# Kernel optimization log

Hardware: AMD Instinct MI355X
Metric: run time of the kernel (lower is better)

Reference implementation:

```python
import jax, jax.numpy as jnp
import numpy as np

N, E, IN_C, HID, OUT_C = 50000, 800000, 128, 64, 64
NEG_SLOPE = 0.2
BN_EPS = 1e-5


def _gat(x, edges, W, a_src, a_dst, b):
    """PyG-style GATConv: linear -> per-head attention logits -> softmax over
    incoming edges (self-loops added, as in PyG default) -> weighted scatter-add."""
    n = x.shape[0]
    H, C = a_src.shape
    xw = (x @ W).reshape(n, H, C)                      # [N,H,C]
    loop = jnp.arange(n)
    src = jnp.concatenate([edges[0], loop])            # [E+N]
    dst = jnp.concatenate([edges[1], loop])
    al_s = jnp.sum(xw * a_src, axis=-1)                # [N,H]
    al_d = jnp.sum(xw * a_dst, axis=-1)
    e = jax.nn.leaky_relu(al_s[src] + al_d[dst], NEG_SLOPE)   # [E+N,H]
    emax = jax.ops.segment_max(e, dst, num_segments=n)        # stable softmax per target
    w = jnp.exp(e - emax[dst])
    denom = jax.ops.segment_sum(w, dst, num_segments=n)
    alpha = w / (denom[dst] + 1e-16)                   # [E+N,H]
    msg = xw[src] * alpha[:, :, None]                  # [E+N,H,C]
    out = jax.ops.segment_sum(msg, dst, num_segments=n)       # [N,H,C]
    return out.reshape(n, H * C) + b


def _bn(x, g, be):
    # BatchNorm1d training-mode forward: biased batch statistics over nodes.
    m = jnp.mean(x, axis=0)
    v = jnp.mean((x - m) ** 2, axis=0)
    return (x - m) * jax.lax.rsqrt(v + BN_EPS) * g + be


def setup_inputs() -> dict:
    key = jax.random.key(0)
    ks = jax.random.split(key, 20)
    p = lambda k, s: (jax.random.normal(k, s, jnp.float32) * 0.1)
    return {
        "x": jax.random.normal(ks[0], (1, N, IN_C), jnp.float32),
        "adj": jax.random.randint(ks[1], (2, E), 0, N),
        # conv1: in=128 -> hidden=64, heads=2 (concat -> 128)
        "W1": p(ks[2], (IN_C, 2 * HID)), "as1": p(ks[3], (2, HID)), "ad1": p(ks[4], (2, HID)), "b1": jnp.zeros((2 * HID,), jnp.float32),
        "g1": jnp.ones((2 * HID,), jnp.float32), "be1": jnp.zeros((2 * HID,), jnp.float32),
        # conv2: 128 -> 64, heads=2
        "W2": p(ks[5], (2 * HID, 2 * HID)), "as2": p(ks[6], (2, HID)), "ad2": p(ks[7], (2, HID)), "b2": jnp.zeros((2 * HID,), jnp.float32),
        "g2": jnp.ones((2 * HID,), jnp.float32), "be2": jnp.zeros((2 * HID,), jnp.float32),
        # conv3: 128 -> 64, heads=1
        "W3": p(ks[8], (2 * HID, OUT_C)), "as3": p(ks[9], (1, OUT_C)), "ad3": p(ks[10], (1, OUT_C)), "b3": jnp.zeros((OUT_C,), jnp.float32),
        "g3": jnp.ones((OUT_C,), jnp.float32), "be3": jnp.zeros((OUT_C,), jnp.float32),
    }


def reference(x, adj, W1, as1, ad1, b1, g1, be1, W2, as2, ad2, b2, g2, be2, W3, as3, ad3, b3, g3, be3):
    x0 = x[0]                                          # squeeze batch dim
    x1 = _bn(jax.nn.relu(_gat(x0, adj, W1, as1, ad1, b1)), g1, be1)   # [N,128]
    x2 = _bn(jax.nn.relu(_gat(x1, adj, W2, as2, ad2, b2)), g2, be2)   # [N,128]
    x3 = _bn(jax.nn.relu(_gat(x2, adj, W3, as3, ad3, b3)), g3, be3)   # [N,64]
    return jnp.concatenate([x1, x2, x3], axis=-1)      # [N,320]
```

## Files before the change

kernel.cpp:

```cpp
#include <hip/hip_runtime.h>

typedef unsigned int uint;
typedef unsigned short ushort;


static __device__ __forceinline__ ushort bf16_rne(float x) {
    uint u = __float_as_uint(x);
    return (ushort)((u + 0x7fffu + ((u >> 16) & 1u)) >> 16);
}
static __device__ __forceinline__ float bf16_f(ushort h) {
    return __uint_as_float(((uint)h) << 16);
}

__global__ __launch_bounds__(256) void k_bcount(const int* __restrict__ dst, int e,
                                                int* __restrict__ bcntp) {
    __shared__ int h[512];
    int tid = threadIdx.x;
    h[tid] = 0;
    h[tid + 256] = 0;
    __syncthreads();
    int stride = gridDim.x * 256;
    for (int i = blockIdx.x * 256 + tid; i < e; i += stride)
        atomicAdd(&h[dst[i] >> 7], 1);
    __syncthreads();
    if (h[tid]) atomicAdd(&bcntp[tid * 16], h[tid]);
    if (h[tid + 256]) atomicAdd(&bcntp[(tid + 256) * 16], h[tid + 256]);
}

__global__ __launch_bounds__(512) void k_bscan(const int* __restrict__ bcntp,
                                               int* __restrict__ bbase,
                                               int* __restrict__ bcurp, int nb, int n,
                                               int total, int* __restrict__ row_start) {
    __shared__ int s[512];
    int tid = threadIdx.x;
    int v = 0;
    if (tid < nb) v = bcntp[tid * 16] + min(128, n - (tid << 7));
    s[tid] = v;
    __syncthreads();
    for (int off = 1; off < 512; off <<= 1) {
        int t = (tid >= off) ? s[tid - off] : 0;
        __syncthreads();
        s[tid] += t;
        __syncthreads();
    }
    if (tid < nb) {
        int excl = s[tid] - v;
        bbase[tid] = excl;
        bcurp[tid * 16] = excl;
    }
    if (tid == 0) {
        bbase[nb] = total;
        row_start[n] = total;
    }
}

__global__ __launch_bounds__(512) void k_bscatter(const int* __restrict__ src,
                                                  const int* __restrict__ dst, int e, int n,
                                                  int* __restrict__ bcurp,
                                                  int* __restrict__ pk) {
    __shared__ int hcnt[512], bstart[512], bcursor[512], gbase[512];
    __shared__ int stage[8192];
    int tid = threadIdx.x;
    int total = e + n;
    int nchunk = (total + 8191) >> 13;
    for (int c = blockIdx.x; c < nchunk; c += gridDim.x) {
        int base = c << 13;
        int cnt = min(8192, total - base);
        hcnt[tid] = 0;
        __syncthreads();
        for (int j = tid; j < cnt; j += 512) {
            int i = base + j;
            int d = (i < e) ? dst[i] : (i - e);
            atomicAdd(&hcnt[d >> 7], 1);
        }
        __syncthreads();
        int v = hcnt[tid];
        bstart[tid] = v;
        __syncthreads();
        for (int off = 1; off < 512; off <<= 1) {
            int t = (tid >= off) ? bstart[tid - off] : 0;
            __syncthreads();
            bstart[tid] += t;
            __syncthreads();
        }
        int excl = bstart[tid] - v;
        __syncthreads();
        bstart[tid] = excl;
        bcursor[tid] = excl;
        if (v) gbase[tid] = atomicAdd(&bcurp[tid * 16], v);
        __syncthreads();
        for (int j = tid; j < cnt; j += 512) {
            int i = base + j;
            int d, sv;
            if (i < e) { d = dst[i]; sv = src[i]; }
            else       { d = i - e; sv = d; }
            uint b = (uint)(d >> 7);
            int r = atomicAdd(&bcursor[b], 1);
            stage[r] = (int)((b << 23) | ((uint)(d & 127) << 16) | (uint)sv);
        }
        __syncthreads();
        for (int j = tid; j < cnt; j += 512) {
            int p = stage[j];
            int b = (int)(((uint)p) >> 23);
            pk[gbase[b] + (j - bstart[b])] = p;
        }
        __syncthreads();
    }
}

__global__ __launch_bounds__(256) void k_bfill(const int* __restrict__ pk,
                                               const int* __restrict__ bbase, int n,
                                               int* __restrict__ row_start,
                                               int* __restrict__ col) {
    int b = blockIdx.x;
    int s0 = bbase[b], s1 = bbase[b + 1];
    int seg = s1 - s0;
    int node0 = b << 7;
    int nn = min(128, n - node0);
    int tid = threadIdx.x;
    __shared__ int cnt[128], scn[128];
    __shared__ int colst[4608];
    if (tid < 128) cnt[tid] = 0;
    __syncthreads();
    for (int j = tid; j < seg; j += 256)
        atomicAdd(&cnt[(pk[s0 + j] >> 16) & 127], 1);
    __syncthreads();
    int myc = 0;
    if (tid < 128) { myc = cnt[tid]; scn[tid] = myc; }
    __syncthreads();
    for (int off = 1; off < 128; off <<= 1) {
        int t = (tid >= off && tid < 128) ? scn[tid - off] : 0;
        __syncthreads();
        if (tid < 128) scn[tid] += t;
        __syncthreads();
    }
    int excl = 0;
    if (tid < 128) excl = scn[tid] - myc;
    if (tid < nn) row_start[node0 + tid] = s0 + excl;
    __syncthreads();
    if (tid < 128) cnt[tid] = excl;
    __syncthreads();
    bool big = seg > 4608;
    for (int j = tid; j < seg; j += 256) {
        int p = pk[s0 + j];
        int r = atomicAdd(&cnt[(p >> 16) & 127], 1);
        if (big) col[s0 + r] = p & 0xffff;
        else colst[r] = p & 0xffff;
    }
    if (!big) {
        __syncthreads();
        for (int j = tid; j < seg; j += 256) col[s0 + j] = colst[j];
    }
}

typedef __attribute__((ext_vector_type(8))) short short8;
typedef __attribute__((ext_vector_type(4))) float float4v;

template <int F, int H, bool BN>
__global__ __launch_bounds__(256) void k_gemm(const float* __restrict__ A,
                                              const float* __restrict__ W,
                                              const float* __restrict__ sc,
                                              const float* __restrict__ sh,
                                              const float* __restrict__ asrc,
                                              const float* __restrict__ adst,
                                              ushort* __restrict__ xwb,
                                              float* __restrict__ al_s,
                                              float* __restrict__ al_d, int M) {
    constexpr int K = 128;
    constexpr int NT = F / 16;
    __shared__ __align__(16) ushort Ahi[64][40], Alo[64][40];
    __shared__ __align__(16) ushort Whi[F][40], Wlo[F][40];
    int tid = threadIdx.x;
    int wave = tid >> 6, lane = tid & 63;
    int quad = lane >> 4, l15 = lane & 15;
    int rowBase = blockIdx.x * 64;

    float4v acc[NT];
#pragma unroll
    for (int t = 0; t < NT; t++) acc[t] = (float4v){0.f, 0.f, 0.f, 0.f};

    for (int k0 = 0; k0 < K; k0 += 32) {
        {
            int kk = tid & 31, rg = tid >> 5;
            float scv = BN ? sc[k0 + kk] : 1.f;
            float shv = BN ? sh[k0 + kk] : 0.f;
#pragma unroll
            for (int i = 0; i < 8; i++) {
                int r = rg + i * 8;
                int grow = rowBase + r;
                float a = (grow < M) ? A[(long long)grow * K + k0 + kk] : 0.f;
                if (BN) a = fmaf(a, scv, shv);
                ushort hi = bf16_rne(a);
                ushort lo = bf16_rne(a - bf16_f(hi));
                Ahi[r][kk] = hi;
                Alo[r][kk] = lo;
            }
        }
        if (F == 128) {
            int n = tid & 127, kg = tid >> 7;
#pragma unroll
            for (int j = 0; j < 16; j++) {
                int kk = kg + j * 2;
                float w = W[(long long)(k0 + kk) * F + n];
                ushort hi = bf16_rne(w);
                ushort lo = bf16_rne(w - bf16_f(hi));
                Whi[n][kk] = hi;
                Wlo[n][kk] = lo;
            }
        } else {
            int n = tid & 63, kg = tid >> 6;
#pragma unroll
            for (int j = 0; j < 8; j++) {
                int kk = kg + j * 4;
                float w = W[(long long)(k0 + kk) * F + n];
                ushort hi = bf16_rne(w);
                ushort lo = bf16_rne(w - bf16_f(hi));
                Whi[n][kk] = hi;
                Wlo[n][kk] = lo;
            }
        }
        __syncthreads();

        short8 ah = *(const short8*)&Ahi[wave * 16 + l15][quad * 8];
        short8 al = *(const short8*)&Alo[wave * 16 + l15][quad * 8];
#pragma unroll
        for (int t = 0; t < NT; t++) {
            short8 bh = *(const short8*)&Whi[t * 16 + l15][quad * 8];
            short8 bl = *(const short8*)&Wlo[t * 16 + l15][quad * 8];
            acc[t] = __builtin_amdgcn_mfma_f32_16x16x32_bf16(ah, bh, acc[t], 0, 0, 0);
            acc[t] = __builtin_amdgcn_mfma_f32_16x16x32_bf16(ah, bl, acc[t], 0, 0, 0);
            acc[t] = __builtin_amdgcn_mfma_f32_16x16x32_bf16(al, bh, acc[t], 0, 0, 0);
        }
        __syncthreads();
    }

    float asl[NT], adl[NT];
#pragma unroll
    for (int t = 0; t < NT; t++) {
        asl[t] = asrc[t * 16 + l15];
        adl[t] = adst[t * 16 + l15];
    }
#pragma unroll
    for (int r = 0; r < 4; r++) {
        int grow = rowBase + wave * 16 + quad * 4 + r;
        if (grow < M) {
#pragma unroll
            for (int t = 0; t < NT; t++)
                xwb[(long long)grow * F + t * 16 + l15] = bf16_rne(acc[t][r]);
        }
        float ps0 = 0.f, pd0 = 0.f, ps1 = 0.f, pd1 = 0.f;
#pragma unroll
        for (int t = 0; t < NT; t++) {
            float v = acc[t][r];
            if (H == 2 && t >= NT / 2) {
                ps1 = fmaf(v, asl[t], ps1);
                pd1 = fmaf(v, adl[t], pd1);
            } else {
                ps0 = fmaf(v, asl[t], ps0);
                pd0 = fmaf(v, adl[t], pd0);
            }
        }
#pragma unroll
        for (int off = 1; off < 16; off <<= 1) {
            ps0 += __shfl_xor(ps0, off);
            pd0 += __shfl_xor(pd0, off);
            if (H == 2) {
                ps1 += __shfl_xor(ps1, off);
                pd1 += __shfl_xor(pd1, off);
            }
        }
        if (l15 == 0 && grow < M) {
            al_s[grow * H + 0] = ps0;
            al_d[grow * H + 0] = pd0;
            if (H == 2) {
                al_s[grow * H + 1] = ps1;
                al_d[grow * H + 1] = pd1;
            }
        }
    }
}

template <int F, int H>
__global__ __launch_bounds__(256) void k_agg(const uint* __restrict__ xwb,
                      const float* __restrict__ al_s,
                      const float* __restrict__ al_d, const int* __restrict__ row_start,
                      const int* __restrict__ col, const float* __restrict__ bias,
                      float* __restrict__ y, int n) {
    int wid = (blockIdx.x * blockDim.x + threadIdx.x) >> 6;
    int lane = threadIdx.x & 63;
    if (wid >= n) return;
    int beg = row_start[wid], end = row_start[wid + 1];

    float ald[H];
#pragma unroll
    for (int h = 0; h < H; h++) ald[h] = al_d[wid * H + h];

    if (end - beg <= 64) {
        int nb = end - beg;
        int s_c = 0;
        float ev0 = -1e30f, ev1 = -1e30f;
        if (lane < nb) {
            s_c = col[beg + lane];
            if (H == 2) {
                float2 av = ((const float2*)al_s)[s_c];
                float e0 = av.x + ald[0];
                float e1 = av.y + ald[1];
                ev0 = (e0 >= 0.f) ? e0 : 0.2f * e0;
                ev1 = (e1 >= 0.f) ? e1 : 0.2f * e1;
            } else {
                float e0 = al_s[s_c] + ald[0];
                ev0 = (e0 >= 0.f) ? e0 : 0.2f * e0;
            }
        }
        float m0 = ev0, m1 = ev1;
#pragma unroll
        for (int off = 32; off; off >>= 1) {
            m0 = fmaxf(m0, __shfl_xor(m0, off));
            if (H == 2) m1 = fmaxf(m1, __shfl_xor(m1, off));
        }
        float x0 = (lane < nb) ? __expf(ev0 - m0) : 0.f;
        float x1 = (H == 2 && lane < nb) ? __expf(ev1 - m1) : 0.f;
        float l0 = x0, l1 = x1;
#pragma unroll
        for (int off = 32; off; off >>= 1) {
            l0 += __shfl_xor(l0, off);
            if (H == 2) l1 += __shfl_xor(l1, off);
        }
        float a0 = x0 / (l0 + 1e-16f);
        float a1 = (H == 2) ? x1 / (l1 + 1e-16f) : a0;

        float accv0 = 0.f, accv1 = 0.f, accv2 = 0.f, accv3 = 0.f;
        const uint2* xw2 = (const uint2*)xwb;

        if (F == 128) {
            int li = lane & 31;
            int half = lane >> 5;
            bool head0 = (li < 16);
            for (int j = 0; j < nb; j += 16) {
                int rr[8];
                float alq[8];
#pragma unroll
                for (int q = 0; q < 8; q++) {
                    int e = j + 2 * q + half;
                    rr[q] = __shfl(s_c, e);
                    float aa = __shfl(a0, e);
                    float bb = __shfl(a1, e);
                    alq[q] = (H == 2) ? (head0 ? aa : bb) : aa;
                }
                uint2 uu[8];
#pragma unroll
                for (int q = 0; q < 8; q++)
                    uu[q] = xw2[(rr[q] << 5) + li];
#pragma unroll
                for (int q = 0; q < 8; q++) {
                    accv0 = fmaf(alq[q], __uint_as_float(uu[q].x << 16), accv0);
                    accv1 = fmaf(alq[q], __uint_as_float(uu[q].x & 0xffff0000u), accv1);
                    accv2 = fmaf(alq[q], __uint_as_float(uu[q].y << 16), accv2);
                    accv3 = fmaf(alq[q], __uint_as_float(uu[q].y & 0xffff0000u), accv3);
                }
            }
            accv0 += __shfl_xor(accv0, 32);
            accv1 += __shfl_xor(accv1, 32);
            accv2 += __shfl_xor(accv2, 32);
            accv3 += __shfl_xor(accv3, 32);
            if (li == lane) {
                float4 o;
                o.x = fmaxf(accv0 + bias[4 * li + 0], 0.f);
                o.y = fmaxf(accv1 + bias[4 * li + 1], 0.f);
                o.z = fmaxf(accv2 + bias[4 * li + 2], 0.f);
                o.w = fmaxf(accv3 + bias[4 * li + 3], 0.f);
                ((float4*)y)[(long long)wid * 32 + li] = o;
            }
        } else {
            int li = lane & 15;
            int g = lane >> 4;
            for (int j = 0; j < nb; j += 32) {
                int rr[8];
                float alq[8];
#pragma unroll
                for (int q = 0; q < 8; q++) {
                    int e = j + 4 * q + g;
                    rr[q] = __shfl(s_c, e);
                    alq[q] = __shfl(a0, e);
                }
                uint2 uu[8];
#pragma unroll
                for (int q = 0; q < 8; q++)
                    uu[q] = xw2[(rr[q] << 4) + li];
#pragma unroll
                for (int q = 0; q < 8; q++) {
                    accv0 = fmaf(alq[q], __uint_as_float(uu[q].x << 16), accv0);
                    accv1 = fmaf(alq[q], __uint_as_float(uu[q].x & 0xffff0000u), accv1);
                    accv2 = fmaf(alq[q], __uint_as_float(uu[q].y << 16), accv2);
                    accv3 = fmaf(alq[q], __uint_as_float(uu[q].y & 0xffff0000u), accv3);
                }
            }
            accv0 += __shfl_xor(accv0, 16); accv0 += __shfl_xor(accv0, 32);
            accv1 += __shfl_xor(accv1, 16); accv1 += __shfl_xor(accv1, 32);
            accv2 += __shfl_xor(accv2, 16); accv2 += __shfl_xor(accv2, 32);
            accv3 += __shfl_xor(accv3, 16); accv3 += __shfl_xor(accv3, 32);
            if (lane < 16) {
                float4 o;
                o.x = fmaxf(accv0 + bias[4 * li + 0], 0.f);
                o.y = fmaxf(accv1 + bias[4 * li + 1], 0.f);
                o.z = fmaxf(accv2 + bias[4 * li + 2], 0.f);
                o.w = fmaxf(accv3 + bias[4 * li + 3], 0.f);
                ((float4*)y)[(long long)wid * 16 + li] = o;
            }
        }
        return;
    }

    float acc0 = 0.f, acc1 = 0.f;
    {
        float m[H], l[H];
#pragma unroll
        for (int h = 0; h < H; h++) {
            m[h] = -1e30f;
            l[h] = 0.f;
        }
        for (int e = beg + lane; e < end; e += 64) {
            int s = col[e];
#pragma unroll
            for (int h = 0; h < H; h++) {
                float ev = al_s[s * H + h] + ald[h];
                ev = (ev >= 0.f) ? ev : 0.2f * ev;
                if (ev > m[h]) {
                    l[h] = l[h] * __expf(m[h] - ev) + 1.f;
                    m[h] = ev;
                } else {
                    l[h] += __expf(ev - m[h]);
                }
            }
        }
#pragma unroll
        for (int off = 32; off; off >>= 1) {
#pragma unroll
            for (int h = 0; h < H; h++) {
                float mo = __shfl_xor(m[h], off);
                float lo = __shfl_xor(l[h], off);
                float mn = fmaxf(m[h], mo);
                l[h] = l[h] * __expf(m[h] - mn) + lo * __expf(mo - mn);
                m[h] = mn;
            }
        }
        float inv[H];
#pragma unroll
        for (int h = 0; h < H; h++) inv[h] = 1.f / (l[h] + 1e-16f);

        for (int base = beg; base < end; base += 64) {
            int nb = min(64, end - base);
            int ec = min(base + lane, end - 1);
            int s = col[ec];
            float a0, a1;
            {
                float av[H];
#pragma unroll
                for (int h = 0; h < H; h++) {
                    float ev = al_s[s * H + h] + ald[h];
                    ev = (ev >= 0.f) ? ev : 0.2f * ev;
                    av[h] = __expf(ev - m[h]) * inv[h];
                }
                a0 = av[0];
                a1 = av[H - 1];
            }
            int j = 0;
            for (; j + 4 <= nb; j += 4) {
                int s0 = __shfl(s, j + 0), s1 = __shfl(s, j + 1);
                int s2 = __shfl(s, j + 2), s3 = __shfl(s, j + 3);
                float q00 = __shfl(a0, j + 0), q01 = __shfl(a1, j + 0);
                float q10 = __shfl(a0, j + 1), q11 = __shfl(a1, j + 1);
                float q20 = __shfl(a0, j + 2), q21 = __shfl(a1, j + 2);
                float q30 = __shfl(a0, j + 3), q31 = __shfl(a1, j + 3);
                float p0, p1, p2, p3;
                if (H == 2) {
                    p0 = (lane < 32) ? q00 : q01;
                    p1 = (lane < 32) ? q10 : q11;
                    p2 = (lane < 32) ? q20 : q21;
                    p3 = (lane < 32) ? q30 : q31;
                } else {
                    p0 = q00; p1 = q10; p2 = q20; p3 = q30;
                }
                if (F == 128) {
                    uint u0 = xwb[(s0 << 6) + lane];
                    uint u1 = xwb[(s1 << 6) + lane];
                    uint u2 = xwb[(s2 << 6) + lane];
                    uint u3 = xwb[(s3 << 6) + lane];
                    acc0 = fmaf(p0, __uint_as_float(u0 << 16), acc0);
                    acc1 = fmaf(p0, __uint_as_float(u0 & 0xffff0000u), acc1);
                    acc0 = fmaf(p1, __uint_as_float(u1 << 16), acc0);
                    acc1 = fmaf(p1, __uint_as_float(u1 & 0xffff0000u), acc1);
                    acc0 = fmaf(p2, __uint_as_float(u2 << 16), acc0);
                    acc1 = fmaf(p2, __uint_as_float(u2 & 0xffff0000u), acc1);
                    acc0 = fmaf(p3, __uint_as_float(u3 << 16), acc0);
                    acc1 = fmaf(p3, __uint_as_float(u3 & 0xffff0000u), acc1);
                } else {
                    int idx = lane >> 1;
                    bool hi = (lane & 1) != 0;
                    uint u0 = xwb[(s0 << 5) + idx];
                    uint u1 = xwb[(s1 << 5) + idx];
                    uint u2 = xwb[(s2 << 5) + idx];
                    uint u3 = xwb[(s3 << 5) + idx];
                    acc0 = fmaf(p0, __uint_as_float(hi ? (u0 & 0xffff0000u) : (u0 << 16)), acc0);
                    acc0 = fmaf(p1, __uint_as_float(hi ? (u1 & 0xffff0000u) : (u1 << 16)), acc0);
                    acc0 = fmaf(p2, __uint_as_float(hi ? (u2 & 0xffff0000u) : (u2 << 16)), acc0);
                    acc0 = fmaf(p3, __uint_as_float(hi ? (u3 & 0xffff0000u) : (u3 << 16)), acc0);
                }
            }
            for (; j < nb; ++j) {
                int sj = __shfl(s, j);
                float q0 = __shfl(a0, j);
                float q1 = __shfl(a1, j);
                float alpha;
                if (H == 2) {
                    alpha = (lane < 32) ? q0 : q1;
                } else {
                    alpha = q0;
                }
                if (F == 128) {
                    uint u = xwb[(sj << 6) + lane];
                    acc0 = fmaf(alpha, __uint_as_float(u << 16), acc0);
                    acc1 = fmaf(alpha, __uint_as_float(u & 0xffff0000u), acc1);
                } else {
                    uint u = xwb[(sj << 5) + (lane >> 1)];
                    acc0 = fmaf(alpha, __uint_as_float((lane & 1) ? (u & 0xffff0000u) : (u << 16)), acc0);
                }
            }
        }
    }

    if (F == 128) {
        float2 o;
        o.x = fmaxf(acc0 + bias[2 * lane], 0.f);
        o.y = fmaxf(acc1 + bias[2 * lane + 1], 0.f);
        ((float2*)y)[(long long)wid * 64 + lane] = o;
    } else {
        y[(long long)wid * 64 + lane] = fmaxf(acc0 + bias[lane], 0.f);
    }
}

template <int F>
__global__ void k_bn_stats(const float* __restrict__ y, float* __restrict__ sums, int n) {
    constexpr int C4 = F / 4;
    constexpr int NPB = 256 / C4;
    int c4 = threadIdx.x % C4;
    int sub = threadIdx.x / C4;
    float4 s = {0, 0, 0, 0}, s2 = {0, 0, 0, 0};
    for (int node = blockIdx.x * NPB + sub; node < n; node += gridDim.x * NPB) {
        float4 v = ((const float4*)y)[node * C4 + c4];
        s.x += v.x; s.y += v.y; s.z += v.z; s.w += v.w;
        s2.x += v.x * v.x; s2.y += v.y * v.y; s2.z += v.z * v.z; s2.w += v.w * v.w;
    }
    __shared__ float4 ls[256], ls2[256];
    ls[threadIdx.x] = s;
    ls2[threadIdx.x] = s2;
    __syncthreads();
    if (sub == 0) {
#pragma unroll
        for (int k = 1; k < NPB; k++) {
            float4 t = ls[c4 + k * C4], t2 = ls2[c4 + k * C4];
            s.x += t.x; s.y += t.y; s.z += t.z; s.w += t.w;
            s2.x += t2.x; s2.y += t2.y; s2.z += t2.z; s2.w += t2.w;
        }
        atomicAdd(&sums[c4 * 4 + 0], s.x);
        atomicAdd(&sums[c4 * 4 + 1], s.y);
        atomicAdd(&sums[c4 * 4 + 2], s.z);
        atomicAdd(&sums[c4 * 4 + 3], s.w);
        atomicAdd(&sums[F + c4 * 4 + 0], s2.x);
        atomicAdd(&sums[F + c4 * 4 + 1], s2.y);
        atomicAdd(&sums[F + c4 * 4 + 2], s2.z);
        atomicAdd(&sums[F + c4 * 4 + 3], s2.w);
    }
}

template <int F>
__global__ void k_bn_prep(const float* __restrict__ sums, const float* __restrict__ g,
                          const float* __restrict__ be, float* __restrict__ sc,
                          float* __restrict__ sh, float invN) {
    int ch = threadIdx.x;
    if (ch < F) {
        float mean = sums[ch] * invN;
        float var = sums[F + ch] * invN - mean * mean;
        float s = g[ch] * rsqrtf(var + 1e-5f);
        sc[ch] = s;
        sh[ch] = be[ch] - mean * s;
    }
}

template <int F>
__global__ void k_bn_apply(const float* __restrict__ y, const float* __restrict__ sc,
                           const float* __restrict__ sh, float* __restrict__ outp, int n) {
    constexpr int C4 = F / 4;
    int t = blockIdx.x * blockDim.x + threadIdx.x;
    if (t >= n * C4) return;
    int node = t / C4, c4 = t % C4;
    float4 v = ((const float4*)y)[t];
    float4 o;
    o.x = v.x * sc[c4 * 4 + 0] + sh[c4 * 4 + 0];
    o.y = v.y * sc[c4 * 4 + 1] + sh[c4 * 4 + 1];
    o.z = v.z * sc[c4 * 4 + 2] + sh[c4 * 4 + 2];
    o.w = v.w * sc[c4 * 4 + 3] + sh[c4 * 4 + 3];
    ((float4*)(outp + (long long)node * 320))[c4] = o;
}

extern "C" void kernel_launch(void* const* d_in, const int* in_sizes, int n_in,
                              void* d_out, int out_size, void* d_ws, size_t ws_size,
                              hipStream_t stream) {
    const float* x   = (const float*)d_in[0];
    const int*   adj = (const int*)d_in[1];
    const float* W1  = (const float*)d_in[2];
    const float* as1 = (const float*)d_in[3];
    const float* ad1 = (const float*)d_in[4];
    const float* b1  = (const float*)d_in[5];
    const float* g1  = (const float*)d_in[6];
    const float* be1 = (const float*)d_in[7];
    const float* W2  = (const float*)d_in[8];
    const float* as2 = (const float*)d_in[9];
    const float* ad2 = (const float*)d_in[10];
    const float* b2  = (const float*)d_in[11];
    const float* g2  = (const float*)d_in[12];
    const float* be2 = (const float*)d_in[13];
    const float* W3  = (const float*)d_in[14];
    const float* as3 = (const float*)d_in[15];
    const float* ad3 = (const float*)d_in[16];
    const float* b3  = (const float*)d_in[17];
    const float* g3  = (const float*)d_in[18];
    const float* be3 = (const float*)d_in[19];
    float* out = (float*)d_out;

    const int N = in_sizes[0] / 128;
    const int E = in_sizes[1] / 2;

    float* ws    = (float*)d_ws;
    float* ybuf  = ws;
    float* al_s  = ybuf + (size_t)N * 128;
    float* al_d  = al_s + (size_t)N * 2;
    float* stats = al_d + (size_t)N * 2;
    float* scb   = stats + 256;
    float* shb   = scb + 128;
    uint* xwb    = (uint*)(shb + 128);
    int* ibase     = (int*)(xwb + (size_t)N * 64);
    int* bcntp     = ibase;
    int* bcurp     = bcntp + 8192;
    int* bbase     = bcurp + 8192;
    int* row_start = ibase + N;
    int* btot      = row_start + (N + 1);
    int* col       = btot + 64;

    int* pk = (int*)ybuf;

    const int* esrc = adj;
    const int* edst = adj + E;

    const int B = 256;
    auto cdiv = [](int a, int b) { return (a + b - 1) / b; };

    const int NB = (N + 127) >> 7;
    hipMemsetAsync(bcntp, 0, 8192 * sizeof(int), stream);
    k_bcount<<<128, 256, 0, stream>>>(edst, E, bcntp);
    k_bscan<<<1, 512, 0, stream>>>(bcntp, bbase, bcurp, NB, N, E + N, row_start);
    int nchunk = (E + N + 8191) >> 13;
    k_bscatter<<<nchunk, 512, 0, stream>>>(esrc, edst, E, N, bcurp, pk);
    k_bfill<<<NB, 256, 0, stream>>>(pk, bbase, N, row_start, col);

    const float invN = 1.f / (float)N;
    ushort* xwb_us = (ushort*)xwb;

    k_gemm<128, 2, false><<<cdiv(N, 64), B, 0, stream>>>(x, W1, nullptr, nullptr,
                                                         as1, ad1, xwb_us, al_s, al_d, N);
    k_agg<128, 2><<<cdiv(N, 4), B, 0, stream>>>(xwb, al_s, al_d, row_start, col, b1, ybuf, N);
    hipMemsetAsync(stats, 0, 256 * sizeof(float), stream);
    k_bn_stats<128><<<256, B, 0, stream>>>(ybuf, stats, N);
    k_bn_prep<128><<<1, 128, 0, stream>>>(stats, g1, be1, scb, shb, invN);
    k_bn_apply<128><<<cdiv(N * 32, B), B, 0, stream>>>(ybuf, scb, shb, out + 0, N);

    k_gemm<128, 2, true><<<cdiv(N, 64), B, 0, stream>>>(ybuf, W2, scb, shb,
                                                        as2, ad2, xwb_us, al_s, al_d, N);
    k_agg<128, 2><<<cdiv(N, 4), B, 0, stream>>>(xwb, al_s, al_d, row_start, col, b2, ybuf, N);
    hipMemsetAsync(stats, 0, 256 * sizeof(float), stream);
    k_bn_stats<128><<<256, B, 0, stream>>>(ybuf, stats, N);
    k_bn_prep<128><<<1, 128, 0, stream>>>(stats, g2, be2, scb, shb, invN);
    k_bn_apply<128><<<cdiv(N * 32, B), B, 0, stream>>>(ybuf, scb, shb, out + 128, N);

    k_gemm<64, 1, true><<<cdiv(N, 64), B, 0, stream>>>(ybuf, W3, scb, shb,
                                                       as3, ad3, xwb_us, al_s, al_d, N);
    k_agg<64, 1><<<cdiv(N, 4), B, 0, stream>>>(xwb, al_s, al_d, row_start, col, b3, ybuf, N);
    hipMemsetAsync(stats, 0, 256 * sizeof(float), stream);
    k_bn_stats<64><<<256, B, 0, stream>>>(ybuf, stats, N);
    k_bn_prep<64><<<1, 64, 0, stream>>>(stats, g3, be3, scb, shb, invN);
    k_bn_apply<64><<<cdiv(N * 16, B), B, 0, stream>>>(ybuf, scb, shb, out + 256, N);
}
```

Before: 461.9 us.

## Pre-split weights to bf16 hi/lo and fold BN affine into weights

A tiny per-layer kernel converts W into transposed bf16 hi/lo arrays once, folding the BatchNorm scale into W and the shift into a per-column constant vector. The GEMM then reads A straight from global memory with vector loads into registers and reads the pre-split weights directly, with no LDS staging and no barriers. For the 128-wide layers each wave handles one head's half of the columns over 32 rows per block. This removes the repeated per-block weight conversion and the BN FMA on A, at the cost of extra small serial launches and uncached repeated global weight reads per wave.

```diff
diff --git a/kernel.cpp b/kernel.cpp
--- a/kernel.cpp
+++ b/kernel.cpp
@@ -153,129 +153,125 @@
     }
 }
 
+template <int F>
+__global__ void k_wconv(const float* __restrict__ W, const float* __restrict__ sc,
+                        const float* __restrict__ sh, int useBN,
+                        ushort* __restrict__ whi, ushort* __restrict__ wlo,
+                        float* __restrict__ cvec) {
+    int n = threadIdx.x;
+    if (n >= F) return;
+    float c = 0.f;
+    for (int k = 0; k < 128; k++) {
+        float w = W[k * F + n];
+        float wsv = useBN ? w * sc[k] : w;
+        if (useBN) c = fmaf(sh[k], w, c);
+        ushort hi = bf16_rne(wsv);
+        ushort lo = bf16_rne(wsv - bf16_f(hi));
+        whi[n * 128 + k] = hi;
+        wlo[n * 128 + k] = lo;
+    }
+    cvec[n] = c;
+}
+
 typedef __attribute__((ext_vector_type(8))) short short8;
 typedef __attribute__((ext_vector_type(4))) float float4v;
 
-template <int F, int H, bool BN>
-__global__ __launch_bounds__(256) void k_gemm(const float* __restrict__ A,
-                                              const float* __restrict__ W,
-                                              const float* __restrict__ sc,
-                                              const float* __restrict__ sh,
-                                              const float* __restrict__ asrc,
-                                              const float* __restrict__ adst,
-                                              ushort* __restrict__ xwb,
-                                              float* __restrict__ al_s,
-                                              float* __restrict__ al_d, int M) {
-    constexpr int K = 128;
-    constexpr int NT = F / 16;
-    __shared__ __align__(16) ushort Ahi[64][40], Alo[64][40];
-    __shared__ __align__(16) ushort Whi[F][40], Wlo[F][40];
+static __device__ __forceinline__ void cvt8(const float4& f0, const float4& f1,
+                                            short8& hi, short8& lo) {
+#define CV8(i, val)                                        \
+    {                                                      \
+        ushort h_ = bf16_rne(val);                         \
+        hi[i] = (short)h_;                                 \
+        lo[i] = (short)bf16_rne((val)-bf16_f(h_));         \
+    }
+    CV8(0, f0.x) CV8(1, f0.y) CV8(2, f0.z) CV8(3, f0.w)
+    CV8(4, f1.x) CV8(5, f1.y) CV8(6, f1.z) CV8(7, f1.w)
+#undef CV8
+}
+
+template <int F, int H>
+__global__ __launch_bounds__(256) void k_gemm2(const float* __restrict__ A,
+                                               const ushort* __restrict__ whi,
+                                               const ushort* __restrict__ wlo,
+                                               const float* __restrict__ cvec,
+                                               const float* __restrict__ asrc,
+                                               const float* __restrict__ adst,
+                                               ushort* __restrict__ xwb,
+                                               float* __restrict__ al_s,
+                                               float* __restrict__ al_d, int M) {
+    constexpr bool SPLIT = (F == 128);
+    constexpr int RPB = SPLIT ? 32 : 64;
     int tid = threadIdx.x;
     int wave = tid >> 6, lane = tid & 63;
     int quad = lane >> 4, l15 = lane & 15;
-    int rowBase = blockIdx.x * 64;
-
-    float4v acc[NT];
-#pragma unroll
-    for (int t = 0; t < NT; t++) acc[t] = (float4v){0.f, 0.f, 0.f, 0.f};
-
-    for (int k0 = 0; k0 < K; k0 += 32) {
-        {
-            int kk = tid & 31, rg = tid >> 5;
-            float scv = BN ? sc[k0 + kk] : 1.f;
-            float shv = BN ? sh[k0 + kk] : 0.f;
-#pragma unroll
-            for (int i = 0; i < 8; i++) {
-                int r = rg + i * 8;
-                int grow = rowBase + r;
-                float a = (grow < M) ? A[(long long)grow * K + k0 + kk] : 0.f;
-                if (BN) a = fmaf(a, scv, shv);
-                ushort hi = bf16_rne(a);
-                ushort lo = bf16_rne(a - bf16_f(hi));
-                Ahi[r][kk] = hi;
-                Alo[r][kk] = lo;
-            }
-        }
-        if (F == 128) {
-            int n = tid & 127, kg = tid >> 7;
-#pragma unroll
-            for (int j = 0; j < 16; j++) {
-                int kk = kg + j * 2;
-                float w = W[(long long)(k0 + kk) * F + n];
-                ushort hi = bf16_rne(w);
-                ushort lo = bf16_rne(w - bf16_f(hi));
-                Whi[n][kk] = hi;
-                Wlo[n][kk] = lo;
-            }
-        } else {
-            int n = tid & 63, kg = tid >> 6;
-#pragma unroll
-            for (int j = 0; j < 8; j++) {
-                int kk = kg + j * 4;
-                float w = W[(long long)(k0 + kk) * F + n];
-                ushort hi = bf16_rne(w);
-                ushort lo = bf16_rne(w - bf16_f(hi));
-                Whi[n][kk] = hi;
-                Wlo[n][kk] = lo;
-            }
-        }
-        __syncthreads();
-
-        short8 ah = *(const short8*)&Ahi[wave * 16 + l15][quad * 8];
-        short8 al = *(const short8*)&Alo[wave * 16 + l15][quad * 8];
-#pragma unroll
-        for (int t = 0; t < NT; t++) {
-            short8 bh = *(const short8*)&Whi[t * 16 + l15][quad * 8];
-            short8 bl = *(const short8*)&Wlo[t * 16 + l15][quad * 8];
+    int rg = SPLIT ? (wave >> 1) : wave;
+    int half = SPLIT ? (wave & 1) : 0;
+    int base = blockIdx.x * RPB + rg * 16;
+    int coff = half * 64;
+
+    float4v acc[4];
+#pragma unroll
+    for (int t = 0; t < 4; t++) acc[t] = (float4v){0.f, 0.f, 0.f, 0.f};
+
+    int arow = base + l15;
+    bool aval = (arow < M);
+    const float* Ap = A + (long long)arow * 128;
+
+#pragma unroll
+    for (int k0 = 0; k0 < 128; k0 += 32) {
+        float4 f0 = {0.f, 0.f, 0.f, 0.f}, f1 = {0.f, 0.f, 0.f, 0.f};
+        if (aval) {
+            f0 = *(const float4*)(Ap + k0 + quad * 8);
+            f1 = *(const float4*)(Ap + k0 + quad * 8 + 4);
+        }
+        short8 ah, al;
+        cvt8(f0, f1, ah, al);
+#pragma unroll
+        for (int t = 0; t < 4; t++) {
+            int n = coff + t * 16 + l15;
+            short8 bh = *(const short8*)&whi[n * 128 + k0 + quad * 8];
+            short8 bl = *(const short8*)&wlo[n * 128 + k0 + quad * 8];
             acc[t] = __builtin_amdgcn_mfma_f32_16x16x32_bf16(ah, bh, acc[t], 0, 0, 0);
             acc[t] = __builtin_amdgcn_mfma_f32_16x16x32_bf16(ah, bl, acc[t], 0, 0, 0);
             acc[t] = __builtin_amdgcn_mfma_f32_16x16x32_bf16(al, bh, acc[t], 0, 0, 0);
         }
-        __syncthreads();
-    }
-
-    float asl[NT], adl[NT];
-#pragma unroll
-    for (int t = 0; t < NT; t++) {
-        asl[t] = asrc[t * 16 + l15];
-        adl[t] = adst[t * 16 + l15];
+    }
+
+    float cv[4], asl[4], adl[4];
+#pragma unroll
+    for (int t = 0; t < 4; t++) {
+        int n = coff + t * 16 + l15;
+        cv[t] = cvec[n];
+        asl[t] = asrc[n];
+        adl[t] = adst[n];
     }
 #pragma unroll
     for (int r = 0; r < 4; r++) {
-        int grow = rowBase + wave * 16 + quad * 4 + r;
+        int grow = base + quad * 4 + r;
+        float v0 = acc[0][r] + cv[0];
+        float v1 = acc[1][r] + cv[1];
+        float v2 = acc[2][r] + cv[2];
+        float v3 = acc[3][r] + cv[3];
         if (grow < M) {
-#pragma unroll
-            for (int t = 0; t < NT; t++)
-                xwb[(long long)grow * F + t * 16 + l15] = bf16_rne(acc[t][r]);
-        }
-        float ps0 = 0.f, pd0 = 0.f, ps1 = 0.f, pd1 = 0.f;
-#pragma unroll
-        for (int t = 0; t < NT; t++) {
-            float v = acc[t][r];
-            if (H == 2 && t >= NT / 2) {
-                ps1 = fmaf(v, asl[t], ps1);
-                pd1 = fmaf(v, adl[t], pd1);
-            } else {
-                ps0 = fmaf(v, asl[t], ps0);
-                pd0 = fmaf(v, adl[t], pd0);
-            }
-        }
+            ushort* xp = xwb + (long long)grow * F + coff + l15;
+            xp[0] = bf16_rne(v0);
+            xp[16] = bf16_rne(v1);
+            xp[32] = bf16_rne(v2);
+            xp[48] = bf16_rne(v3);
+        }
+        float ps = 0.f, pd = 0.f;
+        ps = fmaf(v0, asl[0], ps); pd = fmaf(v0, adl[0], pd);
+        ps = fmaf(v1, asl[1], ps); pd = fmaf(v1, adl[1], pd);
+        ps = fmaf(v2, asl[2], ps); pd = fmaf(v2, adl[2], pd);
+        ps = fmaf(v3, asl[3], ps); pd = fmaf(v3, adl[3], pd);
 #pragma unroll
         for (int off = 1; off < 16; off <<= 1) {
-            ps0 += __shfl_xor(ps0, off);
-            pd0 += __shfl_xor(pd0, off);
-            if (H == 2) {
-                ps1 += __shfl_xor(ps1, off);
-                pd1 += __shfl_xor(pd1, off);
-            }
+            ps += __shfl_xor(ps, off);
+            pd += __shfl_xor(pd, off);
         }
         if (l15 == 0 && grow < M) {
-            al_s[grow * H + 0] = ps0;
-            al_d[grow * H + 0] = pd0;
-            if (H == 2) {
-                al_s[grow * H + 1] = ps1;
-                al_d[grow * H + 1] = pd1;
-            }
+            al_s[grow * H + half] = ps;
+            al_d[grow * H + half] = pd;
         }
     }
 }
@@ -647,6 +643,18 @@
     int* btot      = row_start + (N + 1);
     int* col       = btot + 64;
 
+    uintptr_t wp = (uintptr_t)(col + (E + N));
+    wp = (wp + 63) & ~(uintptr_t)63;
+    ushort* w1hi = (ushort*)wp;
+    ushort* w1lo = w1hi + 16384;
+    ushort* w2hi = w1lo + 16384;
+    ushort* w2lo = w2hi + 16384;
+    ushort* w3hi = w2lo + 16384;
+    ushort* w3lo = w3hi + 8192;
+    float* c1 = (float*)(w3lo + 8192);
+    float* c2 = c1 + 128;
+    float* c3 = c2 + 128;
+
     int* pk = (int*)ybuf;
 
     const int* esrc = adj;
@@ -654,6 +662,8 @@
 
     const int B = 256;
     auto cdiv = [](int a, int b) { return (a + b - 1) / b; };
+
+    k_wconv<128><<<1, 128, 0, stream>>>(W1, nullptr, nullptr, 0, w1hi, w1lo, c1);
 
     const int NB = (N + 127) >> 7;
     hipMemsetAsync(bcntp, 0, 8192 * sizeof(int), stream);
@@ -666,24 +676,26 @@
     const float invN = 1.f / (float)N;
     ushort* xwb_us = (ushort*)xwb;
 
-    k_gemm<128, 2, false><<<cdiv(N, 64), B, 0, stream>>>(x, W1, nullptr, nullptr,
-                                                         as1, ad1, xwb_us, al_s, al_d, N);
+    k_gemm2<128, 2><<<cdiv(N, 32), B, 0, stream>>>(x, w1hi, w1lo, c1,
+                                                   as1, ad1, xwb_us, al_s, al_d, N);
     k_agg<128, 2><<<cdiv(N, 4), B, 0, stream>>>(xwb, al_s, al_d, row_start, col, b1, ybuf, N);
     hipMemsetAsync(stats, 0, 256 * sizeof(float), stream);
     k_bn_stats<128><<<256, B, 0, stream>>>(ybuf, stats, N);
     k_bn_prep<128><<<1, 128, 0, stream>>>(stats, g1, be1, scb, shb, invN);
+    k_wconv<128><<<1, 128, 0, stream>>>(W2, scb, shb, 1, w2hi, w2lo, c2);
     k_bn_apply<128><<<cdiv(N * 32, B), B, 0, stream>>>(ybuf, scb, shb, out + 0, N);
 
-    k_gemm<128, 2, true><<<cdiv(N, 64), B, 0, stream>>>(ybuf, W2, scb, shb,
-                                                        as2, ad2, xwb_us, al_s, al_d, N);
+    k_gemm2<128, 2><<<cdiv(N, 32), B, 0, stream>>>(ybuf, w2hi, w2lo, c2,
+                                                   as2, ad2, xwb_us, al_s, al_d, N);
     k_agg<128, 2><<<cdiv(N, 4), B, 0, stream>>>(xwb, al_s, al_d, row_start, col, b2, ybuf, N);
     hipMemsetAsync(stats, 0, 256 * sizeof(float), stream);
     k_bn_stats<128><<<256, B, 0, stream>>>(ybuf, stats, N);
     k_bn_prep<128><<<1, 128, 0, stream>>>(stats, g2, be2, scb, shb, invN);
+    k_wconv<64><<<1, 64, 0, stream>>>(W3, scb, shb, 1, w3hi, w3lo, c3);
     k_bn_apply<128><<<cdiv(N * 32, B), B, 0, stream>>>(ybuf, scb, shb, out + 128, N);
 
-    k_gemm<64, 1, true><<<cdiv(N, 64), B, 0, stream>>>(ybuf, W3, scb, shb,
-                                                       as3, ad3, xwb_us, al_s, al_d, N);
+    k_gemm2<64, 1><<<cdiv(N, 64), B, 0, stream>>>(ybuf, w3hi, w3lo, c3,
+                                                  as3, ad3, xwb_us, al_s, al_d, N);
     k_agg<64, 1><<<cdiv(N, 4), B, 0, stream>>>(xwb, al_s, al_d, row_start, col, b3, ybuf, N);
     hipMemsetAsync(stats, 0, 256 * sizeof(float), stream);
     k_bn_stats<64><<<256, B, 0, stream>>>(ybuf, stats, N);
```

Result: slower. 617.6 us (+33.7%).
